# Optimization experiments

Hardware: AMD Instinct MI355X
Metric: run time of the kernel (lower is better)

The kernel has to match this reference:

```python
import jax, jax.numpy as jnp
import numpy as np

B, T, IN, H, N, M = 64, 64, 256, 512, 4096, 128
EPS = 1e-8


def setup_inputs() -> dict:
    key = jax.random.key(0)
    ks = jax.random.split(key, 24)
    s = 0.05
    w = lambda k, shape: jax.random.normal(k, shape, jnp.float32) * s
    return {
        "x": jax.random.normal(ks[0], (B, T, 1, IN), jnp.float32),
        "mem0": jax.random.uniform(ks[1], (B, N, M), jnp.float32) * 0.1,
        "Wx": w(ks[2], (IN, H)),
        "Wr": w(ks[3], (M, H)),
        "bC": jnp.zeros((H,), jnp.float32),
        "r_Wk": w(ks[4], (H, M)), "r_bk": jnp.zeros((M,), jnp.float32),
        "r_Wbeta": w(ks[5], (H, 1)), "r_Wg": w(ks[6], (H, 1)),
        "r_Ws": w(ks[7], (H, 3)), "r_Wgam": w(ks[8], (H, 1)),
        "w_Wk": w(ks[9], (H, M)), "w_bk": jnp.zeros((M,), jnp.float32),
        "w_Wbeta": w(ks[10], (H, 1)), "w_Wg": w(ks[11], (H, 1)),
        "w_Ws": w(ks[12], (H, 3)), "w_Wgam": w(ks[13], (H, 1)),
        "w_We": w(ks[14], (H, M)), "w_Wa": w(ks[15], (H, M)),
    }


def _address(h, w_prev, mem, Wk, bk, Wbeta, Wg, Ws, Wgam):
    # h: [B,H], w_prev: [B,N], mem: [B,N,M]
    k = jnp.tanh(h @ Wk + bk)                      # [B,M]
    beta = jax.nn.softplus(h @ Wbeta)              # [B,1]
    g = jax.nn.sigmoid(h @ Wg)                     # [B,1]
    s = jax.nn.softmax(h @ Ws, axis=-1)            # [B,3]
    gamma = 1.0 + jax.nn.softplus(h @ Wgam)        # [B,1]
    # cosine similarity content addressing
    dot = jnp.einsum('bnm,bm->bn', mem, k)         # [B,N]
    mnorm = jnp.linalg.norm(mem, axis=-1)          # [B,N]
    knorm = jnp.linalg.norm(k, axis=-1, keepdims=True)  # [B,1]
    wc = jax.nn.softmax(beta * dot / (mnorm * knorm + EPS), axis=-1)
    wg = g * wc + (1.0 - g) * w_prev               # [B,N]
    # circular shift with 3 taps {-1, 0, +1}
    wt = (s[:, 0:1] * jnp.roll(wg, -1, axis=1)
          + s[:, 1:2] * wg
          + s[:, 2:3] * jnp.roll(wg, 1, axis=1))
    wp = (wt + EPS) ** gamma                        # sharpen
    return wp / jnp.sum(wp, axis=-1, keepdims=True)


def reference(x, mem0, Wx, Wr, bC,
              r_Wk, r_bk, r_Wbeta, r_Wg, r_Ws, r_Wgam,
              w_Wk, w_bk, w_Wbeta, w_Wg, w_Ws, w_Wgam, w_We, w_Wa):
    xt = x.reshape(B, T, -1).transpose(1, 0, 2)    # [T,B,IN]
    w0 = jnp.zeros((B, N), jnp.float32).at[0, 0].set(1.0)
    h0 = jnp.zeros((B, H), jnp.float32)

    def step(carry, x_t):
        mem, wr, ww, h = carry
        # write to memory using previous hidden and ww (erase then add)
        e = jax.nn.sigmoid(h @ w_We)               # [B,M]
        a = jnp.tanh(h @ w_Wa)                     # [B,M]
        mem = mem * (1.0 - ww[:, :, None] * e[:, None, :]) \
              + ww[:, :, None] * a[:, None, :]     # [B,N,M]
        # read
        r = jnp.einsum('bn,bnm->bm', wr, mem)      # [B,M]
        # controller step
        h = jnp.tanh(x_t @ Wx + r @ Wr + bC)       # [B,H]
        # new addressing weights
        wr = _address(h, wr, mem, r_Wk, r_bk, r_Wbeta, r_Wg, r_Ws, r_Wgam)
        ww = _address(h, ww, mem, w_Wk, w_bk, w_Wbeta, w_Wg, w_Ws, w_Wgam)
        return (mem, wr, ww, h), None

    (mem, wr, ww, h), _ = jax.lax.scan(step, (mem0, w0, w0, h0), xt)
    return h                                       # last hidden state [B,H]
```

## Files before the change

kernel.cpp:

```cpp
#include <hip/hip_runtime.h>
#include <math.h>

#define BB 64
#define TT 64
#define INDIM 256
#define HH 512
#define NN 4096
#define MM 128
#define SS 16
#define ROWS 256
#define EPSF 1e-8f

__device__ __forceinline__ float sigmoidf_(float x){ return 1.f/(1.f+expf(-x)); }
__device__ __forceinline__ float softplusf_(float x){ return (x>20.f)? x : log1pf(expf(x)); }

__device__ __forceinline__ void unpack2(unsigned u, float& lo, float& hi){
  lo = __uint_as_float(u << 16);
  hi = __uint_as_float(u & 0xffff0000u);
}
__device__ __forceinline__ unsigned pack2(float a, float b){
  unsigned ua = __float_as_uint(a), ub = __float_as_uint(b);
  ua += 0x7fffu + ((ua >> 16) & 1u);
  ub += 0x7fffu + ((ub >> 16) & 1u);
  return (ua >> 16) | (ub & 0xffff0000u);
}

__global__ __launch_bounds__(256) void kCvt(const float* __restrict__ src,
                                            uint4* __restrict__ dst){
  const size_t i = (size_t)blockIdx.x*blockDim.x + threadIdx.x;
  const float4 f0 = *(const float4*)(src + i*8);
  const float4 f1 = *(const float4*)(src + i*8 + 4);
  uint4 q;
  q.x = pack2(f0.x, f0.y); q.y = pack2(f0.z, f0.w);
  q.z = pack2(f1.x, f1.y); q.w = pack2(f1.z, f1.w);
  dst[i] = q;
}

__global__ __launch_bounds__(512) void kPre(const float* __restrict__ x,
                                            const float* __restrict__ Wx,
                                            const float* __restrict__ bC,
                                            float* __restrict__ xwx){
  const int bt = blockIdx.x, t = threadIdx.x;
  __shared__ float xs[INDIM];
  if (t < INDIM) xs[t] = x[(size_t)bt*INDIM + t];
  __syncthreads();
  float acc = bC[t];
  #pragma unroll 4
  for (int i=0;i<INDIM;++i) acc += xs[i]*Wx[(size_t)i*HH + t];
  xwx[(size_t)bt*HH + t] = acc;
}

__global__ __launch_bounds__(256) void kA(
    const float* __restrict__ eG, const float* __restrict__ aG,
    const float* __restrict__ wrG, const float* __restrict__ wwG,
    uint4* __restrict__ mem, float* __restrict__ rpart, float* __restrict__ mnormG)
{
  const int b = blockIdx.y;
  const int n0 = blockIdx.x * ROWS;
  const int t = threadIdx.x;
  const int grp = t >> 4, lane = t & 15;
  const int m0 = lane * 8;
  float ev[8], av[8];
  {
    const float4 e0 = *(const float4*)(eG + b*MM + m0);
    const float4 e1 = *(const float4*)(eG + b*MM + m0 + 4);
    const float4 a0 = *(const float4*)(aG + b*MM + m0);
    const float4 a1 = *(const float4*)(aG + b*MM + m0 + 4);
    ev[0]=e0.x; ev[1]=e0.y; ev[2]=e0.z; ev[3]=e0.w;
    ev[4]=e1.x; ev[5]=e1.y; ev[6]=e1.z; ev[7]=e1.w;
    av[0]=a0.x; av[1]=a0.y; av[2]=a0.z; av[3]=a0.w;
    av[4]=a1.x; av[5]=a1.y; av[6]=a1.z; av[7]=a1.w;
  }
  float racc[8];
  #pragma unroll
  for (int j=0;j<8;++j) racc[j]=0.f;
  __shared__ float lr[16][128];
  const size_t rowbase = ((size_t)b*NN + n0) * (MM/8);
  for (int rr=0; rr<16; ++rr){
    const int n = n0 + rr*16 + grp;
    const float wwv = wwG[b*NN+n];
    const float wrv = wrG[b*NN+n];
    uint4* mp = mem + rowbase + (size_t)(rr*16+grp)*(MM/8) + lane;
    uint4 q = *mp;
    float v[8];
    unpack2(q.x, v[0], v[1]); unpack2(q.y, v[2], v[3]);
    unpack2(q.z, v[4], v[5]); unpack2(q.w, v[6], v[7]);
    float sq = 0.f;
    #pragma unroll
    for (int j=0;j<8;++j){
      v[j] = v[j]*(1.f - wwv*ev[j]) + wwv*av[j];
      racc[j] += wrv*v[j];
      sq += v[j]*v[j];
    }
    q.x = pack2(v[0],v[1]); q.y = pack2(v[2],v[3]);
    q.z = pack2(v[4],v[5]); q.w = pack2(v[6],v[7]);
    *mp = q;
    #pragma unroll
    for (int msk=1; msk<16; msk<<=1) sq += __shfl_xor(sq, msk);
    if (lane==0) mnormG[b*NN+n] = sqrtf(sq);
  }
  #pragma unroll
  for (int j=0;j<8;++j) lr[grp][m0+j] = racc[j];
  __syncthreads();
  if (t < MM){
    float s=0.f;
    #pragma unroll
    for (int g=0; g<16; ++g) s += lr[g][t];
    rpart[((size_t)b*SS + blockIdx.x)*MM + t] = s;
  }
}

__global__ __launch_bounds__(1024) void kB(
    const float* __restrict__ xwx, int tstep,
    const float* __restrict__ Wr,
    const float* __restrict__ rWk, const float* __restrict__ rbk,
    const float* __restrict__ rWbeta, const float* __restrict__ rWg,
    const float* __restrict__ rWs, const float* __restrict__ rWgam,
    const float* __restrict__ wWk, const float* __restrict__ wbk,
    const float* __restrict__ wWbeta, const float* __restrict__ wWg,
    const float* __restrict__ wWs, const float* __restrict__ wWgam,
    const float* __restrict__ wWe, const float* __restrict__ wWa,
    const float* __restrict__ rpart,
    float* __restrict__ hG, float* __restrict__ krG, float* __restrict__ kwG,
    float* __restrict__ eG, float* __restrict__ aG, float* __restrict__ scal)
{
  const int b = blockIdx.x, t = threadIdx.x;
  __shared__ float rs[MM], hs[HH], ks[2*MM], sd[14], hd[8][128];
  if (t < MM){
    float s=0.f;
    #pragma unroll
    for (int i=0;i<SS;++i) s += rpart[((size_t)b*SS+i)*MM + t];
    rs[t]=s;
  }
  __syncthreads();
  if (t < HH){
    float acc = xwx[((size_t)b*TT + tstep)*HH + t];
    #pragma unroll 4
    for (int m=0;m<MM;++m) acc += rs[m]*Wr[(size_t)m*HH + t];
    float hv = tanhf(acc);
    hs[t]=hv; hG[(size_t)b*HH+t]=hv;
  }
  __syncthreads();
  {
    const int q = t >> 7, m = t & 127;
    const int head = q & 3, jh = q >> 2;
    const float* W = (head==0)? rWk : (head==1)? wWk : (head==2)? wWe : wWa;
    float acc = 0.f;
    const int j0 = jh*256;
    #pragma unroll 4
    for (int j=j0; j<j0+256; ++j) acc += hs[j]*W[(size_t)j*MM + m];
    hd[q][m] = acc;
  }
  __syncthreads();
  if (t < 512){
    const int q = t >> 7, m = t & 127;
    float acc = hd[q][m] + hd[q+4][m];
    if (q==0){ float v=tanhf(acc + rbk[m]); ks[m]=v;    krG[b*MM+m]=v; }
    else if (q==1){ float v=tanhf(acc + wbk[m]); ks[MM+m]=v; kwG[b*MM+m]=v; }
    else if (q==2){ eG[b*MM+m]=sigmoidf_(acc); }
    else          { aG[b*MM+m]=tanhf(acc); }
  }
  __syncthreads();
  {
    const int wv = t>>6, ln = t&63;
    if (wv < 14){
      const int jj = wv;
      float acc=0.f;
      if (jj==6 || jj==13){
        const int o = (jj==6)? 0 : MM;
        const float v1=ks[o+ln], v2=ks[o+64+ln];
        acc = v1*v1 + v2*v2;
      } else {
        const int j2 = (jj<7)? jj : jj-7;
        const bool rd = (jj<7);
        const float* W; int C, c;
        switch (j2){
          case 0: W = rd? rWbeta : wWbeta; C=1; c=0; break;
          case 1: W = rd? rWg   : wWg;    C=1; c=0; break;
          case 2: W = rd? rWgam : wWgam;  C=1; c=0; break;
          default: W = rd? rWs  : wWs;    C=3; c=j2-3; break;
        }
        for (int j=ln; j<HH; j+=64) acc += hs[j]*W[j*C + c];
      }
      #pragma unroll
      for (int msk=1; msk<64; msk<<=1) acc += __shfl_xor(acc, msk);
      if (ln==0) sd[jj]=acc;
    }
  }
  __syncthreads();
  if (t==0){
    float* sc = scal + b*16;
    sc[0] = softplusf_(sd[0]);
    sc[1] = sigmoidf_(sd[1]);
    sc[2] = 1.f + softplusf_(sd[2]);
    {
      float mx = fmaxf(sd[3], fmaxf(sd[4], sd[5]));
      float e0=expf(sd[3]-mx), e1=expf(sd[4]-mx), e2=expf(sd[5]-mx);
      float inv=1.f/(e0+e1+e2);
      sc[3]=e0*inv; sc[4]=e1*inv; sc[5]=e2*inv;
    }
    sc[6] = sqrtf(sd[6]);
    sc[8]  = softplusf_(sd[7]);
    sc[9]  = sigmoidf_(sd[8]);
    sc[10] = 1.f + softplusf_(sd[9]);
    {
      float mx = fmaxf(sd[10], fmaxf(sd[11], sd[12]));
      float e0=expf(sd[10]-mx), e1=expf(sd[11]-mx), e2=expf(sd[12]-mx);
      float inv=1.f/(e0+e1+e2);
      sc[11]=e0*inv; sc[12]=e1*inv; sc[13]=e2*inv;
    }
    sc[14] = sqrtf(sd[13]);
  }
}

__global__ __launch_bounds__(256) void kC(
    const uint4* __restrict__ mem,
    const float* __restrict__ krG, const float* __restrict__ kwG,
    float* __restrict__ dotrG, float* __restrict__ dotwG)
{
  const int b = blockIdx.y;
  const int n0 = blockIdx.x * ROWS;
  const int t = threadIdx.x, grp=t>>4, lane=t&15;
  const int m0 = lane*8;
  float krv[8], kwv[8];
  {
    const float4 k0 = *(const float4*)(krG + b*MM + m0);
    const float4 k1 = *(const float4*)(krG + b*MM + m0 + 4);
    const float4 w0 = *(const float4*)(kwG + b*MM + m0);
    const float4 w1 = *(const float4*)(kwG + b*MM + m0 + 4);
    krv[0]=k0.x; krv[1]=k0.y; krv[2]=k0.z; krv[3]=k0.w;
    krv[4]=k1.x; krv[5]=k1.y; krv[6]=k1.z; krv[7]=k1.w;
    kwv[0]=w0.x; kwv[1]=w0.y; kwv[2]=w0.z; kwv[3]=w0.w;
    kwv[4]=w1.x; kwv[5]=w1.y; kwv[6]=w1.z; kwv[7]=w1.w;
  }
  const size_t rowbase = ((size_t)b*NN + n0) * (MM/8);
  for (int rr=0; rr<16; ++rr){
    const int n = n0 + rr*16 + grp;
    const uint4 q = mem[rowbase + (size_t)(rr*16+grp)*(MM/8) + lane];
    float v[8];
    unpack2(q.x, v[0], v[1]); unpack2(q.y, v[2], v[3]);
    unpack2(q.z, v[4], v[5]); unpack2(q.w, v[6], v[7]);
    float dr=0.f, dw=0.f;
    #pragma unroll
    for (int j=0;j<8;++j){ dr += v[j]*krv[j]; dw += v[j]*kwv[j]; }
    #pragma unroll
    for (int msk=1; msk<16; msk<<=1){
      dr += __shfl_xor(dr, msk);
      dw += __shfl_xor(dw, msk);
    }
    if (lane==0){ dotrG[b*NN+n]=dr; dotwG[b*NN+n]=dw; }
  }
}

__device__ __forceinline__ float blockSum256(float v, volatile float* sc){
  #pragma unroll
  for (int m=1;m<64;m<<=1) v += __shfl_xor(v,m);
  __syncthreads();
  if ((threadIdx.x&63)==0) sc[threadIdx.x>>6]=v;
  __syncthreads();
  return sc[0]+sc[1]+sc[2]+sc[3];
}
__device__ __forceinline__ float blockMax256(float v, volatile float* sc){
  #pragma unroll
  for (int m=1;m<64;m<<=1) v = fmaxf(v, __shfl_xor(v,m));
  __syncthreads();
  if ((threadIdx.x&63)==0) sc[threadIdx.x>>6]=v;
  __syncthreads();
  return fmaxf(fmaxf(sc[0],sc[1]), fmaxf(sc[2],sc[3]));
}

__global__ __launch_bounds__(256) void kD(
    const float* __restrict__ dotrG, const float* __restrict__ dotwG,
    const float* __restrict__ mnormG, const float* __restrict__ scal,
    float* __restrict__ wrG, float* __restrict__ wwG)
{
  const int b = blockIdx.x, head = blockIdx.y, t = threadIdx.x;
  __shared__ float wg[NN];
  __shared__ float sc[4];
  const float* dot = head? dotwG : dotrG;
  float* wv = head? wwG : wrG;
  const float* sb = scal + b*16 + head*8;
  const float beta=sb[0], g=sb[1], gamma=sb[2];
  const float s0=sb[3], s1=sb[4], s2=sb[5], knorm=sb[6];
  float sim[16]; float mx = -1e30f;
  #pragma unroll
  for (int i=0;i<16;++i){
    const int n = i*256 + t;
    const float d  = dot[(size_t)b*NN+n];
    const float mn = mnormG[(size_t)b*NN+n];
    sim[i] = beta*d/(mn*knorm + EPSF);
    mx = fmaxf(mx, sim[i]);
  }
  mx = blockMax256(mx, sc);
  float sum=0.f;
  #pragma unroll
  for (int i=0;i<16;++i){ sim[i]=expf(sim[i]-mx); sum += sim[i]; }
  sum = blockSum256(sum, sc);
  const float inv = 1.f/sum;
  #pragma unroll
  for (int i=0;i<16;++i){
    const int n = i*256 + t;
    wg[n] = g*sim[i]*inv + (1.f-g)*wv[(size_t)b*NN+n];
  }
  __syncthreads();
  float wp[16]; float ps=0.f;
  #pragma unroll
  for (int i=0;i<16;++i){
    const int n = i*256 + t;
    const float wt = s0*wg[(n+1)&(NN-1)] + s1*wg[n] + s2*wg[(n-1)&(NN-1)];
    wp[i] = powf(wt + EPSF, gamma);
    ps += wp[i];
  }
  ps = blockSum256(ps, sc);
  const float ip = 1.f/ps;
  #pragma unroll
  for (int i=0;i<16;++i){
    const int n = i*256 + t;
    wv[(size_t)b*NN+n] = wp[i]*ip;
  }
}

__global__ void kInit(float* wr, float* ww, float* h, float* e, float* a){
  const int i = blockIdx.x*blockDim.x + threadIdx.x;
  if (i < BB*NN){ const float v = (i==0)? 1.f : 0.f; wr[i]=v; ww[i]=v; }
  if (i < BB*HH) h[i]=0.f;
  if (i < BB*MM){ e[i]=0.5f; a[i]=0.f; }
}
__global__ void kOut(const float* __restrict__ h, float* __restrict__ out){
  const int i = blockIdx.x*blockDim.x + threadIdx.x;
  if (i < BB*HH) out[i]=h[i];
}

extern "C" void kernel_launch(void* const* d_in, const int* in_sizes, int n_in,
                              void* d_out, int out_size, void* d_ws, size_t ws_size,
                              hipStream_t stream)
{
  const float* x     = (const float*)d_in[0];
  const float* mem0  = (const float*)d_in[1];
  const float* Wx    = (const float*)d_in[2];
  const float* Wr    = (const float*)d_in[3];
  const float* bC    = (const float*)d_in[4];
  const float* rWk   = (const float*)d_in[5];
  const float* rbk   = (const float*)d_in[6];
  const float* rWbeta= (const float*)d_in[7];
  const float* rWg   = (const float*)d_in[8];
  const float* rWs   = (const float*)d_in[9];
  const float* rWgam = (const float*)d_in[10];
  const float* wWk   = (const float*)d_in[11];
  const float* wbk   = (const float*)d_in[12];
  const float* wWbeta= (const float*)d_in[13];
  const float* wWg   = (const float*)d_in[14];
  const float* wWs   = (const float*)d_in[15];
  const float* wWgam = (const float*)d_in[16];
  const float* wWe   = (const float*)d_in[17];
  const float* wWa   = (const float*)d_in[18];

  float* ws = (float*)d_ws;
  size_t o = 0;
  uint4* mem   = (uint4*)(ws + o); o += (size_t)BB*NN*MM/2;
  float* wr    = ws + o; o += (size_t)BB*NN;
  float* ww    = ws + o; o += (size_t)BB*NN;
  float* h     = ws + o; o += (size_t)BB*HH;
  float* rpart = ws + o; o += (size_t)BB*SS*MM;
  float* e     = ws + o; o += (size_t)BB*MM;
  float* a     = ws + o; o += (size_t)BB*MM;
  float* kr    = ws + o; o += (size_t)BB*MM;
  float* kw    = ws + o; o += (size_t)BB*MM;
  float* mnorm = ws + o; o += (size_t)BB*NN;
  float* dotr  = ws + o; o += (size_t)BB*NN;
  float* dotw  = ws + o; o += (size_t)BB*NN;
  float* scal  = ws + o; o += (size_t)BB*16;
  float* xwx   = ws + o; o += (size_t)BB*TT*HH;

  kCvt<<<(BB*NN*MM/8)/256, 256, 0, stream>>>(mem0, mem);
  kInit<<<(BB*NN+255)/256, 256, 0, stream>>>(wr, ww, h, e, a);
  kPre<<<BB*TT, 512, 0, stream>>>(x, Wx, bC, xwx);

  for (int t=0; t<TT; ++t){
    kA<<<dim3(SS,BB), 256, 0, stream>>>(e, a, wr, ww, mem, rpart, mnorm);
    kB<<<BB, 1024, 0, stream>>>(xwx, t, Wr,
                               rWk, rbk, rWbeta, rWg, rWs, rWgam,
                               wWk, wbk, wWbeta, wWg, wWs, wWgam, wWe, wWa,
                               rpart, h, kr, kw, e, a, scal);
    if (t < TT-1){
      kC<<<dim3(SS,BB), 256, 0, stream>>>(mem, kr, kw, dotr, dotw);
      kD<<<dim3(BB,2), 256, 0, stream>>>(dotr, dotw, mnorm, scal, wr, ww);
    }
  }
  kOut<<<(BB*HH+255)/256, 256, 0, stream>>>(h, (float*)d_out);
}
```

Before: 5.216 ms.

## Halve rows per block, prefetch memory rows, use fast math and fuse output

Raises the block count for the memory-update and dot kernels by halving the rows each block handles, and software-prefetches the next bf16 memory row while the current one is processed. Address weights are loaded up front. The softmax and sharpening use the fast __expf and __powf intrinsics, the bf16 pack now calls the HIP intrinsic, and the final output is written straight from kB so the kOut launch is dropped. The goal is more latency hiding in the memory-bound kernels and less launch and transcendental cost, at the price of doubling the partial read sums kB must reduce and slightly lower accuracy in the fast math. The rpart buffer size and kB's summation loop follow SS, so the change stays consistent if the workspace is sized with SS.

```diff
diff --git a/kernel.cpp b/kernel.cpp
--- a/kernel.cpp
+++ b/kernel.cpp
@@ -1,4 +1,5 @@
 #include <hip/hip_runtime.h>
+#include <hip/hip_bf16.h>
 #include <math.h>
 
 #define BB 64
@@ -7,8 +8,8 @@
 #define HH 512
 #define NN 4096
 #define MM 128
-#define SS 16
-#define ROWS 256
+#define SS 32
+#define ROWS 128
 #define EPSF 1e-8f
 
 __device__ __forceinline__ float sigmoidf_(float x){ return 1.f/(1.f+expf(-x)); }
@@ -18,11 +19,9 @@
   lo = __uint_as_float(u << 16);
   hi = __uint_as_float(u & 0xffff0000u);
 }
-__device__ __forceinline__ unsigned pack2(float a, float b){
-  unsigned ua = __float_as_uint(a), ub = __float_as_uint(b);
-  ua += 0x7fffu + ((ua >> 16) & 1u);
-  ub += 0x7fffu + ((ub >> 16) & 1u);
-  return (ua >> 16) | (ub & 0xffff0000u);
+__device__ __forceinline__ unsigned packrn(float a, float b){
+  __hip_bfloat162 p = __float22bfloat162_rn(make_float2(a,b));
+  return *reinterpret_cast<unsigned*>(&p);
 }
 
 __global__ __launch_bounds__(256) void kCvt(const float* __restrict__ src,
@@ -31,8 +30,8 @@
   const float4 f0 = *(const float4*)(src + i*8);
   const float4 f1 = *(const float4*)(src + i*8 + 4);
   uint4 q;
-  q.x = pack2(f0.x, f0.y); q.y = pack2(f0.z, f0.w);
-  q.z = pack2(f1.x, f1.y); q.w = pack2(f1.z, f1.w);
+  q.x = packrn(f0.x, f0.y); q.y = packrn(f0.z, f0.w);
+  q.z = packrn(f1.x, f1.y); q.w = packrn(f1.z, f1.w);
   dst[i] = q;
 }
 
@@ -71,33 +70,43 @@
     av[0]=a0.x; av[1]=a0.y; av[2]=a0.z; av[3]=a0.w;
     av[4]=a1.x; av[5]=a1.y; av[6]=a1.z; av[7]=a1.w;
   }
+  float wwv[8], wrv[8];
+  #pragma unroll
+  for (int rr=0; rr<8; ++rr){
+    const int n = n0 + rr*16 + grp;
+    wwv[rr] = wwG[b*NN+n];
+    wrv[rr] = wrG[b*NN+n];
+  }
   float racc[8];
   #pragma unroll
   for (int j=0;j<8;++j) racc[j]=0.f;
   __shared__ float lr[16][128];
-  const size_t rowbase = ((size_t)b*NN + n0) * (MM/8);
-  for (int rr=0; rr<16; ++rr){
+  const size_t base4 = ((size_t)b*NN + n0)*(MM/8) + (size_t)grp*(MM/8) + lane;
+  uint4 q = mem[base4];
+  #pragma unroll
+  for (int rr=0; rr<8; ++rr){
+    uint4 qn;
+    if (rr<7) qn = mem[base4 + (size_t)(rr+1)*16*(MM/8)];
     const int n = n0 + rr*16 + grp;
-    const float wwv = wwG[b*NN+n];
-    const float wrv = wrG[b*NN+n];
-    uint4* mp = mem + rowbase + (size_t)(rr*16+grp)*(MM/8) + lane;
-    uint4 q = *mp;
     float v[8];
     unpack2(q.x, v[0], v[1]); unpack2(q.y, v[2], v[3]);
     unpack2(q.z, v[4], v[5]); unpack2(q.w, v[6], v[7]);
     float sq = 0.f;
+    const float w = wwv[rr], wr_ = wrv[rr];
     #pragma unroll
     for (int j=0;j<8;++j){
-      v[j] = v[j]*(1.f - wwv*ev[j]) + wwv*av[j];
-      racc[j] += wrv*v[j];
+      v[j] = v[j]*(1.f - w*ev[j]) + w*av[j];
+      racc[j] += wr_*v[j];
       sq += v[j]*v[j];
     }
-    q.x = pack2(v[0],v[1]); q.y = pack2(v[2],v[3]);
-    q.z = pack2(v[4],v[5]); q.w = pack2(v[6],v[7]);
-    *mp = q;
+    uint4 q2;
+    q2.x = packrn(v[0],v[1]); q2.y = packrn(v[2],v[3]);
+    q2.z = packrn(v[4],v[5]); q2.w = packrn(v[6],v[7]);
+    mem[base4 + (size_t)rr*16*(MM/8)] = q2;
     #pragma unroll
     for (int msk=1; msk<16; msk<<=1) sq += __shfl_xor(sq, msk);
     if (lane==0) mnormG[b*NN+n] = sqrtf(sq);
+    q = qn;
   }
   #pragma unroll
   for (int j=0;j<8;++j) lr[grp][m0+j] = racc[j];
@@ -122,7 +131,8 @@
     const float* __restrict__ wWe, const float* __restrict__ wWa,
     const float* __restrict__ rpart,
     float* __restrict__ hG, float* __restrict__ krG, float* __restrict__ kwG,
-    float* __restrict__ eG, float* __restrict__ aG, float* __restrict__ scal)
+    float* __restrict__ eG, float* __restrict__ aG, float* __restrict__ scal,
+    float* __restrict__ outG)
 {
   const int b = blockIdx.x, t = threadIdx.x;
   __shared__ float rs[MM], hs[HH], ks[2*MM], sd[14], hd[8][128];
@@ -139,6 +149,7 @@
     for (int m=0;m<MM;++m) acc += rs[m]*Wr[(size_t)m*HH + t];
     float hv = tanhf(acc);
     hs[t]=hv; hG[(size_t)b*HH+t]=hv;
+    if (tstep == TT-1) outG[(size_t)b*HH+t]=hv;
   }
   __syncthreads();
   {
@@ -233,10 +244,13 @@
     kwv[0]=w0.x; kwv[1]=w0.y; kwv[2]=w0.z; kwv[3]=w0.w;
     kwv[4]=w1.x; kwv[5]=w1.y; kwv[6]=w1.z; kwv[7]=w1.w;
   }
-  const size_t rowbase = ((size_t)b*NN + n0) * (MM/8);
-  for (int rr=0; rr<16; ++rr){
+  const size_t base4 = ((size_t)b*NN + n0)*(MM/8) + (size_t)grp*(MM/8) + lane;
+  uint4 q = mem[base4];
+  #pragma unroll
+  for (int rr=0; rr<8; ++rr){
+    uint4 qn;
+    if (rr<7) qn = mem[base4 + (size_t)(rr+1)*16*(MM/8)];
     const int n = n0 + rr*16 + grp;
-    const uint4 q = mem[rowbase + (size_t)(rr*16+grp)*(MM/8) + lane];
     float v[8];
     unpack2(q.x, v[0], v[1]); unpack2(q.y, v[2], v[3]);
     unpack2(q.z, v[4], v[5]); unpack2(q.w, v[6], v[7]);
@@ -249,6 +263,7 @@
       dw += __shfl_xor(dw, msk);
     }
     if (lane==0){ dotrG[b*NN+n]=dr; dotwG[b*NN+n]=dw; }
+    q = qn;
   }
 }
 
@@ -294,7 +309,7 @@
   mx = blockMax256(mx, sc);
   float sum=0.f;
   #pragma unroll
-  for (int i=0;i<16;++i){ sim[i]=expf(sim[i]-mx); sum += sim[i]; }
+  for (int i=0;i<16;++i){ sim[i]=__expf(sim[i]-mx); sum += sim[i]; }
   sum = blockSum256(sum, sc);
   const float inv = 1.f/sum;
   #pragma unroll
@@ -308,7 +323,7 @@
   for (int i=0;i<16;++i){
     const int n = i*256 + t;
     const float wt = s0*wg[(n+1)&(NN-1)] + s1*wg[n] + s2*wg[(n-1)&(NN-1)];
-    wp[i] = powf(wt + EPSF, gamma);
+    wp[i] = __powf(wt + EPSF, gamma);
     ps += wp[i];
   }
   ps = blockSum256(ps, sc);
@@ -325,10 +340,6 @@
   if (i < BB*NN){ const float v = (i==0)? 1.f : 0.f; wr[i]=v; ww[i]=v; }
   if (i < BB*HH) h[i]=0.f;
   if (i < BB*MM){ e[i]=0.5f; a[i]=0.f; }
-}
-__global__ void kOut(const float* __restrict__ h, float* __restrict__ out){
-  const int i = blockIdx.x*blockDim.x + threadIdx.x;
-  if (i < BB*HH) out[i]=h[i];
 }
 
 extern "C" void kernel_launch(void* const* d_in, const int* in_sizes, int n_in,
@@ -381,11 +392,10 @@
     kB<<<BB, 1024, 0, stream>>>(xwx, t, Wr,
                                rWk, rbk, rWbeta, rWg, rWs, rWgam,
                                wWk, wbk, wWbeta, wWg, wWs, wWgam, wWe, wWa,
-                               rpart, h, kr, kw, e, a, scal);
+                               rpart, h, kr, kw, e, a, scal, (float*)d_out);
     if (t < TT-1){
       kC<<<dim3(SS,BB), 256, 0, stream>>>(mem, kr, kw, dotr, dotw);
       kD<<<dim3(BB,2), 256, 0, stream>>>(dotr, dotw, mnorm, scal, wr, ww);
     }
   }
-  kOut<<<(BB*HH+255)/256, 256, 0, stream>>>(h, (float*)d_out);
-}
+}
```

Result: faster. 5.054 ms (-3.1%).
